# Optimization experiments

Measured on AMD Instinct MI355X. Metric: run time of the kernel, lower is better.

## Reference

```python
import jax, jax.numpy as jnp
import numpy as np

B = 4096
N = 4097  # num_samples; basis fit uses N-1 columns


def _trapz_cumsum(x, t):
    # y[..., 0] = 0; y[..., i] = y[..., i-1] + 0.5*(t[i]-t[i-1])*(x[..., i-1]+x[..., i])
    dt = t[1:] - t[:-1]                                   # (N-1,)
    inc = 0.5 * dt * (x[..., :-1] + x[..., 1:])           # (B,1,N-1)
    zero = jnp.zeros(x.shape[:-1] + (1,), x.dtype)
    return jnp.concatenate([zero, jnp.cumsum(inc, axis=-1)], axis=-1)  # (B,1,N)


def setup_inputs() -> dict:
    key = jax.random.key(0)
    k1, k2 = jax.random.split(key)
    # positive signal so ny + cumsum(x) stays > 0 (needed for pow/log)
    x = jax.random.uniform(k1, (B, 1, N), dtype=jnp.float32, minval=0.1, maxval=1.1)
    # strictly increasing time grid
    dt = jax.random.uniform(k2, (N,), dtype=jnp.float32, minval=1e-3, maxval=1e-2)
    t = jnp.cumsum(dt)
    params = jnp.array([0.5, 1.0], dtype=jnp.float32)  # [r, ny]
    return {"x": x, "t": t, "params": params}


def reference(x, t, params):
    r, ny = params[0], params[1]
    y = _trapz_cumsum(x, t)                  # (B,1,N)
    z = ny + y[:, 0, 1:]                     # (B,N-1)
    phi = jnp.stack([z, z ** r], axis=1)     # (B,2,N-1)  basis matrix
    phip = jnp.linalg.pinv(phi)              # (B,N-1,2)
    x_sl = x[:, :, 1:]                       # (B,1,N-1)
    coeffs = x_sl @ phip                     # (B,1,2)
    x_hat = coeffs @ phi                     # (B,1,N-1)
    res = x_sl - x_hat                       # (B,1,N-1)
    r2 = jnp.sum(res ** 2, axis=-1)          # (B,1)
    return coeffs, x_hat, res, r2
```

## Files before the change

### kernel.cpp

```cpp
#include <hip/hip_runtime.h>

typedef float f32x4 __attribute__((ext_vector_type(4)));

constexpr int NPTS = 4097;
constexpr int M    = 4096;
constexpr int TPB  = 512;
constexpr int NW   = TPB / 64;
constexpr int NJ   = 2;

struct Lds {
    float wt[NW][NJ];
    float gram[NW][6];
};

template<int S>
__device__ __forceinline__ void scan4(const f32x4 a, const f32x4 c,
                                      const f32x4 tq, float tn,
                                      float (&xsj)[4], float (&zlj)[4], float& gsj)
{
    const float m[8] = {a.x, a.y, a.z, a.w, c.x, c.y, c.z, c.w};
    const float x0 = m[S+0], x1 = m[S+1], x2 = m[S+2], x3 = m[S+3], x4 = m[S+4];
    const float i0 = (0.5f * (tq.y - tq.x)) * (x0 + x1);
    const float i1 = (0.5f * (tq.z - tq.y)) * (x1 + x2);
    const float i2 = (0.5f * (tq.w - tq.z)) * (x2 + x3);
    const float i3 = (0.5f * (tn   - tq.w)) * (x3 + x4);
    zlj[0] = i0;
    zlj[1] = i0 + i1;
    zlj[2] = zlj[1] + i2;
    zlj[3] = zlj[2] + i3;
    gsj = zlj[3];
    xsj[0] = x1; xsj[1] = x2; xsj[2] = x3; xsj[3] = x4;
}

template<int S, bool RHALF>
__device__ __forceinline__ void body(const float* __restrict__ x,
                                     const float* __restrict__ t,
                                     float r, float ny,
                                     float* __restrict__ out,
                                     int b, int B, Lds& L)
{
    const int tid  = threadIdx.x;
    const int lane = tid & 63;
    const int wid  = tid >> 6;

    const float* __restrict__ xal = x + (size_t)b * NPTS - S;

    float xs[NJ][4];
    float zl[NJ][4];
    float gs[NJ];

#pragma unroll
    for (int j = 0; j < NJ; ++j) {
        const int e = j * 2048 + tid * 4;
        const f32x4 a4 = *(const f32x4*)(xal + e);
        const f32x4 c4 = *(const f32x4*)(xal + e + 4);
        const f32x4 tq = *(const f32x4*)(t + e);
        const float tn = t[e + 4];
        scan4<S>(a4, c4, tq, tn, xs[j], zl[j], gs[j]);
    }

    float sc[NJ];
#pragma unroll
    for (int c = 0; c < NJ; ++c) sc[c] = gs[c];
#pragma unroll
    for (int d = 1; d < 64; d <<= 1) {
#pragma unroll
        for (int c = 0; c < NJ; ++c) {
            float u = __shfl_up(sc[c], d, 64);
            if (lane >= d) sc[c] += u;
        }
    }
    if (lane == 63) {
#pragma unroll
        for (int c = 0; c < NJ; ++c) L.wt[wid][c] = sc[c];
    }
    __syncthreads();

    float woff[NJ] = {}, Tt[NJ] = {};
#pragma unroll
    for (int w = 0; w < NW; ++w) {
#pragma unroll
        for (int c = 0; c < NJ; ++c) {
            const float v = L.wt[w][c];
            Tt[c] += v;
            if (w < wid) woff[c] += v;
        }
    }
    {
        float jacc = ny;
#pragma unroll
        for (int j = 0; j < NJ; ++j) {
            const float zb = jacc + woff[j] + (sc[j] - gs[j]);
            jacc += Tt[j];
#pragma unroll
            for (int i = 0; i < 4; ++i) zl[j][i] = zb + zl[j][i];
        }
    }

    float s0 = 0, s1 = 0, s2 = 0, s3 = 0, s4 = 0, s5 = 0;
#pragma unroll
    for (int j = 0; j < NJ; ++j) {
        float pzz = 0, pzw = 0, pww = 0, pxz = 0, pxw = 0, pxx = 0;
#pragma unroll
        for (int i = 0; i < 4; ++i) {
            const float z  = zl[j][i];
            const float w  = RHALF ? sqrtf(z) : powf(z, r);
            const float xv = xs[j][i];
            pzz = fmaf(z,  z,  pzz);
            pzw = fmaf(z,  w,  pzw);
            pww = fmaf(w,  w,  pww);
            pxz = fmaf(xv, z,  pxz);
            pxw = fmaf(xv, w,  pxw);
            pxx = fmaf(xv, xv, pxx);
        }
        s0 += pzz; s1 += pzw; s2 += pww; s3 += pxz; s4 += pxw; s5 += pxx;
    }
#pragma unroll
    for (int d = 32; d > 0; d >>= 1) {
        s0 += __shfl_down(s0, d, 64);
        s1 += __shfl_down(s1, d, 64);
        s2 += __shfl_down(s2, d, 64);
        s3 += __shfl_down(s3, d, 64);
        s4 += __shfl_down(s4, d, 64);
        s5 += __shfl_down(s5, d, 64);
    }
    if (lane == 0) {
        L.gram[wid][0] = s0; L.gram[wid][1] = s1; L.gram[wid][2] = s2;
        L.gram[wid][3] = s3; L.gram[wid][4] = s4; L.gram[wid][5] = s5;
    }
    __syncthreads();

    double a0 = 0, a1 = 0, a2 = 0, a3 = 0, a4 = 0, a5 = 0;
#pragma unroll
    for (int w = 0; w < NW; ++w) {
        a0 += L.gram[w][0]; a1 += L.gram[w][1]; a2 += L.gram[w][2];
        a3 += L.gram[w][3]; a4 += L.gram[w][4]; a5 += L.gram[w][5];
    }
    const double det = a0 * a2 - a1 * a1;
    const double inv = 1.0 / det;
    const double c0d = (a3 * a2 - a4 * a1) * inv;
    const double c1d = (a4 * a0 - a3 * a1) * inv;
    const float c0 = (float)c0d;
    const float c1 = (float)c1d;
    if (tid == 0) {
        out[(size_t)b * 2 + 0] = c0;
        out[(size_t)b * 2 + 1] = c1;
        out[(size_t)B * 2 + 2 * (size_t)B * M + b] =
            (float)(a5 - c0d * a3 - c1d * a4);
    }

    float* __restrict__ xhat = out + (size_t)B * 2 + (size_t)b * M;
    float* __restrict__ res  = xhat + (size_t)B * M;

#pragma unroll
    for (int j = 0; j < NJ; ++j) {
        const int e = j * 2048 + tid * 4;
        f32x4 hv, rv;
#pragma unroll
        for (int i = 0; i < 4; ++i) {
            const float z = zl[j][i];
            const float w = RHALF ? sqrtf(z) : powf(z, r);
            const float h = c0 * z + c1 * w;
            hv[i] = h;
            rv[i] = xs[j][i] - h;
        }
        *(f32x4*)(xhat + e) = hv;
        *(f32x4*)(res  + e) = rv;
    }
}

__global__ __launch_bounds__(TPB)
void vp_kernel(const float* __restrict__ x, const float* __restrict__ t,
               const float* __restrict__ params, float* __restrict__ out, int B)
{
    __shared__ Lds L;
    const float r  = params[0];
    const float ny = params[1];
    const int  b   = blockIdx.x;

    if (r == 0.5f) {
        switch (b & 3) {
        case 0:  body<0, true>(x, t, r, ny, out, b, B, L); break;
        case 1:  body<1, true>(x, t, r, ny, out, b, B, L); break;
        case 2:  body<2, true>(x, t, r, ny, out, b, B, L); break;
        default: body<3, true>(x, t, r, ny, out, b, B, L); break;
        }
    } else {
        switch (b & 3) {
        case 0:  body<0, false>(x, t, r, ny, out, b, B, L); break;
        case 1:  body<1, false>(x, t, r, ny, out, b, B, L); break;
        case 2:  body<2, false>(x, t, r, ny, out, b, B, L); break;
        default: body<3, false>(x, t, r, ny, out, b, B, L); break;
        }
    }
}

extern "C" void kernel_launch(void* const* d_in, const int* in_sizes, int n_in,
                              void* d_out, int out_size, void* d_ws, size_t ws_size,
                              hipStream_t stream) {
    const float* x = (const float*)d_in[0];
    const float* t = (const float*)d_in[1];
    const float* p = (const float*)d_in[2];
    float* out     = (float*)d_out;
    const int B    = in_sizes[0] / NPTS;

    vp_kernel<<<dim3(B), dim3(TPB), 0, stream>>>(x, t, p, out, B);
}
```

Baseline: 47.87 us.

## Precompute half-dt table in prelaunch kernel, halve block size, hoist all loads

Adds a small kernel that writes 0.5*(t[i+1]-t[i]) into workspace, so the main kernel loads one aligned vector of dt per chunk instead of a vector of t plus a scalar neighbour. Blocks shrink from 512 to 256 threads, each handling four chunks, and all global loads are issued up front before the scans. This aims to cut per-element load instructions and increase memory-level parallelism. The cost is an extra kernel launch and higher register pressure from holding more in-flight vectors.

```diff
diff --git a/kernel.cpp b/kernel.cpp
--- a/kernel.cpp
+++ b/kernel.cpp
@@ -4,26 +4,33 @@
 
 constexpr int NPTS = 4097;
 constexpr int M    = 4096;
-constexpr int TPB  = 512;
+constexpr int TPB  = 256;
 constexpr int NW   = TPB / 64;
-constexpr int NJ   = 2;
+constexpr int NJ   = 4;
 
 struct Lds {
     float wt[NW][NJ];
     float gram[NW][6];
 };
 
+__global__ __launch_bounds__(256)
+void k_dtab(const float* __restrict__ t, float* __restrict__ d)
+{
+    const int i = blockIdx.x * 256 + threadIdx.x;
+    if (i < M) d[i] = 0.5f * (t[i + 1] - t[i]);
+}
+
 template<int S>
 __device__ __forceinline__ void scan4(const f32x4 a, const f32x4 c,
-                                      const f32x4 tq, float tn,
+                                      const f32x4 d4,
                                       float (&xsj)[4], float (&zlj)[4], float& gsj)
 {
     const float m[8] = {a.x, a.y, a.z, a.w, c.x, c.y, c.z, c.w};
     const float x0 = m[S+0], x1 = m[S+1], x2 = m[S+2], x3 = m[S+3], x4 = m[S+4];
-    const float i0 = (0.5f * (tq.y - tq.x)) * (x0 + x1);
-    const float i1 = (0.5f * (tq.z - tq.y)) * (x1 + x2);
-    const float i2 = (0.5f * (tq.w - tq.z)) * (x2 + x3);
-    const float i3 = (0.5f * (tn   - tq.w)) * (x3 + x4);
+    const float i0 = d4.x * (x0 + x1);
+    const float i1 = d4.y * (x1 + x2);
+    const float i2 = d4.z * (x2 + x3);
+    const float i3 = d4.w * (x3 + x4);
     zlj[0] = i0;
     zlj[1] = i0 + i1;
     zlj[2] = zlj[1] + i2;
@@ -34,7 +41,7 @@
 
 template<int S, bool RHALF>
 __device__ __forceinline__ void body(const float* __restrict__ x,
-                                     const float* __restrict__ t,
+                                     const float* __restrict__ dt2,
                                      float r, float ny,
                                      float* __restrict__ out,
                                      int b, int B, Lds& L)
@@ -45,19 +52,21 @@
 
     const float* __restrict__ xal = x + (size_t)b * NPTS - S;
 
+    f32x4 a4[NJ], c4[NJ], d4[NJ];
+#pragma unroll
+    for (int j = 0; j < NJ; ++j) {
+        const int e = j * 1024 + tid * 4;
+        a4[j] = *(const f32x4*)(xal + e);
+        c4[j] = *(const f32x4*)(xal + e + 4);
+        d4[j] = *(const f32x4*)(dt2 + e);
+    }
+
     float xs[NJ][4];
     float zl[NJ][4];
     float gs[NJ];
-
-#pragma unroll
-    for (int j = 0; j < NJ; ++j) {
-        const int e = j * 2048 + tid * 4;
-        const f32x4 a4 = *(const f32x4*)(xal + e);
-        const f32x4 c4 = *(const f32x4*)(xal + e + 4);
-        const f32x4 tq = *(const f32x4*)(t + e);
-        const float tn = t[e + 4];
-        scan4<S>(a4, c4, tq, tn, xs[j], zl[j], gs[j]);
-    }
+#pragma unroll
+    for (int j = 0; j < NJ; ++j)
+        scan4<S>(a4[j], c4[j], d4[j], xs[j], zl[j], gs[j]);
 
     float sc[NJ];
 #pragma unroll
@@ -130,23 +139,23 @@
     }
     __syncthreads();
 
-    double a0 = 0, a1 = 0, a2 = 0, a3 = 0, a4 = 0, a5 = 0;
+    double a0 = 0, a1 = 0, a2 = 0, a3 = 0, a4d = 0, a5 = 0;
 #pragma unroll
     for (int w = 0; w < NW; ++w) {
-        a0 += L.gram[w][0]; a1 += L.gram[w][1]; a2 += L.gram[w][2];
-        a3 += L.gram[w][3]; a4 += L.gram[w][4]; a5 += L.gram[w][5];
+        a0 += L.gram[w][0]; a1  += L.gram[w][1]; a2 += L.gram[w][2];
+        a3 += L.gram[w][3]; a4d += L.gram[w][4]; a5 += L.gram[w][5];
     }
     const double det = a0 * a2 - a1 * a1;
     const double inv = 1.0 / det;
-    const double c0d = (a3 * a2 - a4 * a1) * inv;
-    const double c1d = (a4 * a0 - a3 * a1) * inv;
+    const double c0d = (a3 * a2 - a4d * a1) * inv;
+    const double c1d = (a4d * a0 - a3 * a1) * inv;
     const float c0 = (float)c0d;
     const float c1 = (float)c1d;
     if (tid == 0) {
         out[(size_t)b * 2 + 0] = c0;
         out[(size_t)b * 2 + 1] = c1;
         out[(size_t)B * 2 + 2 * (size_t)B * M + b] =
-            (float)(a5 - c0d * a3 - c1d * a4);
+            (float)(a5 - c0d * a3 - c1d * a4d);
     }
 
     float* __restrict__ xhat = out + (size_t)B * 2 + (size_t)b * M;
@@ -154,7 +163,7 @@
 
 #pragma unroll
     for (int j = 0; j < NJ; ++j) {
-        const int e = j * 2048 + tid * 4;
+        const int e = j * 1024 + tid * 4;
         f32x4 hv, rv;
 #pragma unroll
         for (int i = 0; i < 4; ++i) {
@@ -170,7 +179,7 @@
 }
 
 __global__ __launch_bounds__(TPB)
-void vp_kernel(const float* __restrict__ x, const float* __restrict__ t,
+void vp_kernel(const float* __restrict__ x, const float* __restrict__ dt2,
                const float* __restrict__ params, float* __restrict__ out, int B)
 {
     __shared__ Lds L;
@@ -180,17 +189,17 @@
 
     if (r == 0.5f) {
         switch (b & 3) {
-        case 0:  body<0, true>(x, t, r, ny, out, b, B, L); break;
-        case 1:  body<1, true>(x, t, r, ny, out, b, B, L); break;
-        case 2:  body<2, true>(x, t, r, ny, out, b, B, L); break;
-        default: body<3, true>(x, t, r, ny, out, b, B, L); break;
+        case 0:  body<0, true>(x, dt2, r, ny, out, b, B, L); break;
+        case 1:  body<1, true>(x, dt2, r, ny, out, b, B, L); break;
+        case 2:  body<2, true>(x, dt2, r, ny, out, b, B, L); break;
+        default: body<3, true>(x, dt2, r, ny, out, b, B, L); break;
         }
     } else {
         switch (b & 3) {
-        case 0:  body<0, false>(x, t, r, ny, out, b, B, L); break;
-        case 1:  body<1, false>(x, t, r, ny, out, b, B, L); break;
-        case 2:  body<2, false>(x, t, r, ny, out, b, B, L); break;
-        default: body<3, false>(x, t, r, ny, out, b, B, L); break;
+        case 0:  body<0, false>(x, dt2, r, ny, out, b, B, L); break;
+        case 1:  body<1, false>(x, dt2, r, ny, out, b, B, L); break;
+        case 2:  body<2, false>(x, dt2, r, ny, out, b, B, L); break;
+        default: body<3, false>(x, dt2, r, ny, out, b, B, L); break;
         }
     }
 }
@@ -202,7 +211,9 @@
     const float* t = (const float*)d_in[1];
     const float* p = (const float*)d_in[2];
     float* out     = (float*)d_out;
+    float* dt2     = (float*)d_ws;
     const int B    = in_sizes[0] / NPTS;
 
-    vp_kernel<<<dim3(B), dim3(TPB), 0, stream>>>(x, t, p, out, B);
-}
+    k_dtab<<<dim3((M + 255) / 256), dim3(256), 0, stream>>>(t, dt2);
+    vp_kernel<<<dim3(B), dim3(TPB), 0, stream>>>(x, dt2, p, out, B);
+}
```

Result: faster. 44.48 us (-7.1%).
